# Optimization experiments

Hardware: AMD Instinct MI355X
Metric: run time of the kernel (lower is better)

## Reference

```python
import jax, jax.numpy as jnp
import numpy as np

# decoded layout constants
NN, NO, SD = 16, 8, 4          # num_neighbors, num_obstacles, state_dim_per_agent
B = 131072                      # batch rows
H1, E, HP, AD = 64, 16, 64, 2   # phi hidden, embed, psi hidden, action dim
D_ROBOT, D_OBST = 0.3, 0.3
B_GAMMA, B_EXPH = 0.05, 1.0
PHI_MIN, PHI_MAX = -2.0, 2.0
A_MAX = 2.0


def setup_inputs() -> dict:
    key = jax.random.key(0)
    kx, kw = jax.random.split(key)
    # x: [count | goal(SD) | NN neighbor rel-states (SD each) | NO obstacle rel-pos (2 each)]
    x = jax.random.normal(kx, (B, 1 + SD + SD * NN + 2 * NO), dtype=jnp.float32) * 2.0
    x = x.at[:, 0].set(float(NN))
    names = [("Wp1n", (SD, H1)), ("bp1n", (H1,)), ("Wp2n", (H1, E)), ("bp2n", (E,)),
             ("Wr1n", (E, H1)), ("br1n", (H1,)), ("Wr2n", (H1, E)), ("br2n", (E,)),
             ("Wp1o", (2, H1)), ("bp1o", (H1,)), ("Wp2o", (H1, E)), ("bp2o", (E,)),
             ("Wr1o", (E, H1)), ("br1o", (H1,)), ("Wr2o", (H1, E)), ("br2o", (E,)),
             ("Wpsi1", (2 * E + SD, HP)), ("bpsi1", (HP,)), ("Wpsi2", (HP, AD)), ("bpsi2", (AD,))]
    ks = jax.random.split(kw, len(names))
    inp = {"x": x}
    for (n, sh), k in zip(names, ks):
        s = 1.0 / np.sqrt(sh[0])  # torch Linear default init scale
        inp[n] = jax.random.uniform(k, sh, jnp.float32, -s, s)
    return inp


def _mlp2(h, W1, b1, W2, b2):
    # Feedforward: activation between layers, linear output
    return jax.nn.relu(h @ W1 + b1) @ W2 + b2


def _deepset(el, Wp1, bp1, Wp2, bp2, Wr1, br1, Wr2, br2):
    # el: [B, n, d] -> phi each element, sum over set, rho
    phi = _mlp2(el, Wp1, bp1, Wp2, bp2)          # [B, n, E]
    return _mlp2(phi.sum(axis=1), Wr1, br1, Wr2, br2)  # [B, E]


def _barrier_sum(P, D):
    # P: [B, n, 2]; APF barrier gamma * P / (|P| * (|P|-D)^exph), summed over n
    nrm = jnp.linalg.norm(P, axis=-1, keepdims=True)   # [B, n, 1]
    H = nrm - D
    return (B_GAMMA * P / (nrm * H ** B_EXPH)).sum(axis=1)  # [B, 2]


def reference(x, Wp1n, bp1n, Wp2n, bp2n, Wr1n, br1n, Wr2n, br2n,
              Wp1o, bp1o, Wp2o, bp2o, Wr1o, br1o, Wr2o, br2o,
              Wpsi1, bpsi1, Wpsi2, bpsi2):
    nb = x.shape[0]
    g = x[:, 1:1 + SD]                                        # goal
    nbr = x[:, 1 + SD:1 + SD + SD * NN].reshape(nb, NN, SD)   # neighbor rel-states
    obs = x[:, 1 + SD + SD * NN:].reshape(nb, NO, 2)          # obstacle rel-pos

    rho_n = _deepset(nbr, Wp1n, bp1n, Wp2n, bp2n, Wr1n, br1n, Wr2n, br2n)
    rho_o = _deepset(obs, Wp1o, bp1o, Wp2o, bp2o, Wr1o, br1o, Wr2o, br2o)

    h = jnp.concatenate([rho_n, rho_o, g], axis=1)            # [B, 2E+SD]
    emp = _mlp2(h, Wpsi1, bpsi1, Wpsi2, bpsi2)                # psi network
    emp = (jnp.tanh(emp) + 1.0) / 2.0 * (PHI_MAX - PHI_MIN) + PHI_MIN  # scale_empty

    bar = _barrier_sum(-nbr[:, :, :2], D_ROBOT) + _barrier_sum(-obs, D_OBST)

    action = emp + bar
    # scale(): divide rows whose inf-norm exceeds a_max
    inv_alpha = jnp.maximum(jnp.max(jnp.abs(action), axis=1, keepdims=True) / A_MAX, 1.0)
    return action / inv_alpha
```

## Files before the change

kernel.cpp:

```cpp
#include <hip/hip_runtime.h>
#include <math.h>


typedef __attribute__((ext_vector_type(8))) _Float16 f16x8;
typedef __attribute__((ext_vector_type(2))) __fp16 fp16x2;
typedef __attribute__((ext_vector_type(4))) float f32x4;

#define XW 85

#define FR_S1N  0
#define FR_S1O  4
#define FR_FN   8
#define FR_FO   16
#define FR_ZN   24
#define FR_ZO   32
#define FR_WG   40
#define FR_PSI2 44
#define FR_SPN  46
#define FR_SPO  50
#define N_FRAGS 54

#define BIG_STR 144
#define L_BIG  0
#define L_BIG2 2304
#define L_OUT  4608
#define L_BAR  4736
#define GRP_LDS 4864
#define NBA_STR 136

#define H16_ONE 0x00003C00u

__device__ __forceinline__ float fast_rcp(float x)  { return __builtin_amdgcn_rcpf(x); }
__device__ __forceinline__ float fast_sqrt(float x) { return __builtin_amdgcn_sqrtf(x); }

__device__ __forceinline__ float two_tanh(float a) {
    float ax = fabsf(a);
    float e = __expf(2.0f * ax);
    float t = 1.0f - 2.0f * fast_rcp(e + 1.0f);
    return copysignf(2.0f * t, a);
}

__device__ __forceinline__ void lds_order() {
    __asm__ __volatile__("" ::: "memory");
}

__device__ __forceinline__ unsigned pk2(float a, float b) {
    union { fp16x2 h; unsigned u; } t;
    t.h = __builtin_amdgcn_cvt_pkrtz(a, b);
    return t.u;
}
__device__ __forceinline__ f16x8 lds_af(const char* area, int stride, int off, int lane) {
    int mm = lane & 15, qq = lane >> 4;
    return *(const f16x8*)(area + mm * stride + off + qq * 16);
}
__device__ __forceinline__ f16x8 load_bh(const _Float16* wsf, int frag, int lane) {
    return ((const f16x8*)(wsf + (size_t)frag * 512))[lane];
}
__device__ __forceinline__ f32x4 cinit(float b) {
    f32x4 c; c[0] = b; c[1] = b; c[2] = b; c[3] = b; return c;
}
__device__ __forceinline__ f32x4 mfma1(f16x8 a, f16x8 b, f32x4 c) {
    return __builtin_amdgcn_mfma_f32_16x16x32_f16(a, b, c, 0, 0, 0);
}

__global__ void bn_prep(const float* __restrict__ Wp1n, const float* __restrict__ Wp2n,
                        const float* __restrict__ Wr1n, const float* __restrict__ Wr2n,
                        const float* __restrict__ Wp1o, const float* __restrict__ Wp2o,
                        const float* __restrict__ Wr1o, const float* __restrict__ Wr2o,
                        const float* __restrict__ Wpsi1, const float* __restrict__ Wpsi2,
                        const float* __restrict__ bp1n, const float* __restrict__ bp1o,
                        const float* __restrict__ bp2n, const float* __restrict__ bp2o,
                        const float* __restrict__ br1n, const float* __restrict__ br1o,
                        const float* __restrict__ br2n, const float* __restrict__ br2o,
                        const float* __restrict__ bpsi1,
                        _Float16* __restrict__ wsf)
{
    int f = blockIdx.x;
    int lane = threadIdx.x;
    int q = lane >> 4, c = lane & 15;

    if (f >= N_FRAGS) {
        float* dst = (float*)(wsf + (size_t)N_FRAGS * 512) + (f - N_FRAGS) * 64;
        if (lane < 64) {
            if (f == N_FRAGS) {
                float s = 0.f;
                for (int e = 0; e < 16; ++e) s = fmaf(bp2n[e], Wr1n[e * 64 + lane], s);
                dst[lane] = 16.f * s + br1n[lane];
            } else if (f == N_FRAGS + 1) {
                float s = 0.f;
                for (int e = 0; e < 16; ++e) s = fmaf(bp2o[e], Wr1o[e * 64 + lane], s);
                dst[lane] = 8.f * s + br1o[lane];
            } else if (f == N_FRAGS + 2) {
                dst[lane] = 16.f * bp1n[lane];
            } else {
                dst[lane] = 8.f * bp1o[lane];
            }
        }
        return;
    }

    _Float16* dstf = wsf + (size_t)f * 512 + lane * 8;

    if (f < 8) {
        const float* W   = (f < 4) ? Wp1n : Wp1o;
        const float* bia = (f < 4) ? bp1n : bp1o;
        int K  = (f < 4) ? 4 : 2;
        int nt = f & 3;
        for (int j = 0; j < 8; ++j) {
            int k = q * 8 + j;
            int n = nt * 16 + c;
            float v = 0.f;
            if (k < K) v = W[k * 64 + n];
            else if (k == K) v = bia[n];
            dstf[j] = (_Float16)v;
        }
    } else if (f < 24) {
        int rel = (f - 8) & 7;
        bool isN = f < 16;
        const float* Wa = isN ? Wp2n : Wp2o;
        const float* Wb = isN ? Wr1n : Wr1o;
        int kk = rel >> 2, nt = rel & 3;
        for (int j = 0; j < 8; ++j) {
            int k = kk * 32 + q * 8 + j;
            int n = nt * 16 + c;
            float s = 0.f;
            for (int e = 0; e < 16; ++e) s = fmaf(Wa[k * 16 + e], Wb[e * 64 + n], s);
            dstf[j] = (_Float16)(0.5f * s);
        }
    } else if (f < 40) {
        int rel = (f - 24) & 7;
        bool isN = f < 32;
        const float* Wa = isN ? Wr2n : Wr2o;
        int roff = isN ? 0 : 16;
        int kk = rel >> 2, nt = rel & 3;
        for (int j = 0; j < 8; ++j) {
            int k = kk * 32 + q * 8 + j;
            int n = nt * 16 + c;
            float s = 0.f;
            for (int e = 0; e < 16; ++e) s = fmaf(Wa[k * 16 + e], Wpsi1[(roff + e) * 64 + n], s);
            dstf[j] = (_Float16)s;
        }
    } else if (f < 44) {
        int nt = f - 40;
        for (int j = 0; j < 8; ++j) {
            int k = q * 8 + j;
            int n = nt * 16 + c;
            float v = 0.f;
            if (k < 4) v = Wpsi1[(32 + k) * 64 + n];
            else if (k == 4) {
                float s = bpsi1[n];
                for (int e = 0; e < 16; ++e) {
                    s = fmaf(br2n[e], Wpsi1[e * 64 + n], s);
                    s = fmaf(br2o[e], Wpsi1[(16 + e) * 64 + n], s);
                }
                v = s;
            }
            dstf[j] = (_Float16)v;
        }
    } else if (f < 46) {
        int kk = f - 44;
        for (int j = 0; j < 8; ++j) {
            int k = kk * 32 + q * 8 + j;
            float v = (c < 2) ? Wpsi2[k * 2 + c] : 0.f;
            dstf[j] = (_Float16)v;
        }
    } else if (f < 50) {
        int nt = f - 46;
        for (int j = 0; j < 8; ++j) {
            int k = q * 8 + j;
            int n = nt * 16 + c;
            dstf[j] = (_Float16)Wp1n[(k & 3) * 64 + n];
        }
    } else {
        int nt = f - 50;
        for (int j = 0; j < 8; ++j) {
            int k = q * 8 + j;
            int n = nt * 16 + c;
            float v = (k < 16) ? Wp1o[(k & 1) * 64 + n] : 0.f;
            dstf[j] = (_Float16)v;
        }
    }
}

__global__ __launch_bounds__(256, 5) void bn_main(
    const float* __restrict__ x, const _Float16* __restrict__ wsf,
    const float* __restrict__ bpsi2,
    float* __restrict__ out, int nb)
{
    __shared__ char smem[4 * GRP_LDS];
    const int lane = threadIdx.x & 63;
    const int wid  = threadIdx.x >> 6;
    const int group = blockIdx.x * 4 + wid;
    const int row0 = group * 16;

    char* Gl   = smem + wid * GRP_LDS;
    char* BIG  = Gl + L_BIG;
    char* BIG2 = Gl + L_BIG2;
    char* OUTA = Gl + L_OUT;
    char* BAR  = Gl + L_BAR;
    char* NBA  = BIG;

    const int m = lane & 15, q = lane >> 4, c = m;
    const float* xg   = x + (size_t)row0 * XW;
    const float* xrow = xg + (size_t)m * XW;

    const float* BFN = (const float*)(wsf + (size_t)N_FRAGS * 512);
    const float* BFO = BFN + 64;
    const float* BSN = BFN + 128;
    const float* BSO = BFN + 192;

    const f32x4 ZC = cinit(0.f);

    {
        int ln5 = lane >> 5;
        int pr  = lane & 31;
        int mm0 = pr >> 1, fp = pr & 1;
        char* db = NBA + mm0 * NBA_STR + fp * 4;
        const float* s0 = xg + (size_t)ln5 * XW + 5 + pr * 2;
        #pragma unroll
        for (int t = 0; t < 8; ++t) {
            const float* s = s0 + (size_t)(2 * t) * XW;
            *(unsigned*)(db + (2 * t + ln5) * 8) = pk2(s[0], s[1]);
        }
    }

    union { f16x8 v; unsigned u[4]; } gA;
    gA.u[0] = pk2(xrow[1], xrow[2]);
    gA.u[1] = pk2(xrow[3], xrow[4]);
    gA.u[2] = H16_ONE;
    gA.u[3] = 0;

    unsigned obs[8];
    #pragma unroll
    for (int t = 0; t < 8; ++t)
        obs[t] = pk2(xrow[69 + 2 * t], xrow[70 + 2 * t]);

    {
        float bx = 0.f, by = 0.f;
        #pragma unroll
        for (int i = 0; i < 4; ++i) {
            int n = 4 * q + i;
            float px = -xrow[5 + 4 * n], py = -xrow[6 + 4 * n];
            float nrm = fast_sqrt(px * px + py * py);
            float coef = 0.05f * fast_rcp(nrm * (nrm - 0.3f));
            bx = fmaf(coef, px, bx);
            by = fmaf(coef, py, by);
        }
        #pragma unroll
        for (int i = 0; i < 2; ++i) {
            int o = 2 * q + i;
            float px = -xrow[69 + 2 * o], py = -xrow[70 + 2 * o];
            float nrm = fast_sqrt(px * px + py * py);
            float coef = 0.05f * fast_rcp(nrm * (nrm - 0.3f));
            bx = fmaf(coef, px, bx);
            by = fmaf(coef, py, by);
        }
        bx += __shfl_xor(bx, 16); by += __shfl_xor(by, 16);
        bx += __shfl_xor(bx, 32); by += __shfl_xor(by, 32);
        if (q == 0) { float2 bb; bb.x = bx; bb.y = by; *(float2*)(BAR + m * 8) = bb; }
    }

    {
        f16x8 Bspo[4], Bs1o[4];
        #pragma unroll
        for (int nt = 0; nt < 4; ++nt) {
            Bspo[nt] = load_bh(wsf, FR_SPO + nt, lane);
            Bs1o[nt] = load_bh(wsf, FR_S1O + nt, lane);
        }
        union { f16x8 v; unsigned u[4]; } Apo;
        Apo.u[0] = q == 0 ? obs[0] : (q == 1 ? obs[4] : 0u);
        Apo.u[1] = q == 0 ? obs[1] : (q == 1 ? obs[5] : 0u);
        Apo.u[2] = q == 0 ? obs[2] : (q == 1 ? obs[6] : 0u);
        Apo.u[3] = q == 0 ? obs[3] : (q == 1 ? obs[7] : 0u);

        f32x4 accS[4], accA[4];
        #pragma unroll
        for (int nt = 0; nt < 4; ++nt) {
            accS[nt] = mfma1(Apo.v, Bspo[nt], cinit(BSO[nt * 16 + c]));
            accA[nt] = cinit(0.f);
        }
        union { f16x8 v; unsigned u[4]; } A;
        A.u[1] = H16_ONE; A.u[2] = 0; A.u[3] = 0;
        #pragma unroll
        for (int oo = 0; oo < 8; ++oo) {
            A.u[0] = obs[oo];
            #pragma unroll
            for (int nt = 0; nt < 4; ++nt) {
                f32x4 cc = mfma1(A.v, Bs1o[nt], ZC);
                #pragma unroll
                for (int reg = 0; reg < 4; ++reg)
                    accA[nt][reg] += fabsf(cc[reg]);
            }
        }
        #pragma unroll
        for (int nt = 0; nt < 4; ++nt)
            #pragma unroll
            for (int reg = 0; reg < 4; ++reg)
                *(_Float16*)(BIG2 + (q * 4 + reg) * BIG_STR + (nt * 16 + c) * 2)
                    = (_Float16)(accS[nt][reg] + accA[nt][reg]);
    }
    lds_order();

    {
        f16x8 Bspn[4], Bs1n[4];
        #pragma unroll
        for (int nt = 0; nt < 4; ++nt) {
            Bspn[nt] = load_bh(wsf, FR_SPN + nt, lane);
            Bs1n[nt] = load_bh(wsf, FR_S1N + nt, lane);
        }
        const int m8 = m * 8;
        union { f16x8 v; uint2 h[2]; } Ap0, Ap1;
        Ap0.h[0] = *(const uint2*)(NBA + (2 * q) * NBA_STR + m8);
        Ap0.h[1] = *(const uint2*)(NBA + (2 * q + 1) * NBA_STR + m8);
        Ap1.h[0] = *(const uint2*)(NBA + (2 * q + 8) * NBA_STR + m8);
        Ap1.h[1] = *(const uint2*)(NBA + (2 * q + 9) * NBA_STR + m8);

        f32x4 accS[4], accA[4];
        #pragma unroll
        for (int nt = 0; nt < 4; ++nt) {
            accS[nt] = mfma1(Ap1.v, Bspn[nt],
                       mfma1(Ap0.v, Bspn[nt], cinit(BSN[nt * 16 + c])));
            accA[nt] = cinit(0.f);
        }
        union { f16x8 v; unsigned u[4]; uint2 h[2]; } A;
        A.u[2] = H16_ONE; A.u[3] = 0;
        #pragma unroll
        for (int mm = 0; mm < 16; ++mm) {
            A.h[0] = *(const uint2*)(NBA + mm * NBA_STR + m8);
            #pragma unroll
            for (int nt = 0; nt < 4; ++nt) {
                f32x4 cc = mfma1(A.v, Bs1n[nt], ZC);
                #pragma unroll
                for (int reg = 0; reg < 4; ++reg)
                    accA[nt][reg] += fabsf(cc[reg]);
            }
        }
        lds_order();
        #pragma unroll
        for (int nt = 0; nt < 4; ++nt)
            #pragma unroll
            for (int reg = 0; reg < 4; ++reg)
                *(_Float16*)(BIG + (q * 4 + reg) * BIG_STR + (nt * 16 + c) * 2)
                    = (_Float16)(accS[nt][reg] + accA[nt][reg]);
    }
    lds_order();

    {
        f16x8 An0 = lds_af(BIG,  BIG_STR, 0, lane);
        f16x8 An1 = lds_af(BIG,  BIG_STR, 64, lane);
        f16x8 Ao0 = lds_af(BIG2, BIG_STR, 0, lane);
        f16x8 Ao1 = lds_af(BIG2, BIG_STR, 64, lane);
        #pragma unroll
        for (int nt = 0; nt < 4; ++nt) {
            f16x8 Bn0 = load_bh(wsf, FR_FN + nt, lane);
            f16x8 Bn1 = load_bh(wsf, FR_FN + 4 + nt, lane);
            f32x4 cn = mfma1(An0, Bn0, cinit(BFN[nt * 16 + c]));
            cn = mfma1(An1, Bn1, cn);
            f16x8 Bo0 = load_bh(wsf, FR_FO + nt, lane);
            f16x8 Bo1 = load_bh(wsf, FR_FO + 4 + nt, lane);
            f32x4 co = mfma1(Ao0, Bo0, cinit(BFO[nt * 16 + c]));
            co = mfma1(Ao1, Bo1, co);
            #pragma unroll
            for (int reg = 0; reg < 4; ++reg) {
                *(_Float16*)(BIG + (q * 4 + reg) * BIG_STR + (nt * 16 + c) * 2)
                    = (_Float16)fmaxf(cn[reg], 0.f);
                *(_Float16*)(BIG2 + (q * 4 + reg) * BIG_STR + (nt * 16 + c) * 2)
                    = (_Float16)fmaxf(co[reg], 0.f);
            }
        }
    }
    lds_order();

    {
        f16x8 An0 = lds_af(BIG,  BIG_STR, 0, lane);
        f16x8 An1 = lds_af(BIG,  BIG_STR, 64, lane);
        f16x8 Ao0 = lds_af(BIG2, BIG_STR, 0, lane);
        f16x8 Ao1 = lds_af(BIG2, BIG_STR, 64, lane);
        #pragma unroll
        for (int nt = 0; nt < 4; ++nt) {
            f16x8 Bg  = load_bh(wsf, FR_WG + nt, lane);
            f16x8 Bn0 = load_bh(wsf, FR_ZN + nt, lane);
            f16x8 Bn1 = load_bh(wsf, FR_ZN + 4 + nt, lane);
            f16x8 Bo0 = load_bh(wsf, FR_ZO + nt, lane);
            f16x8 Bo1 = load_bh(wsf, FR_ZO + 4 + nt, lane);
            f32x4 cc = mfma1(gA.v, Bg, ZC);
            cc = mfma1(An0, Bn0, cc);
            cc = mfma1(An1, Bn1, cc);
            cc = mfma1(Ao0, Bo0, cc);
            cc = mfma1(Ao1, Bo1, cc);
            #pragma unroll
            for (int reg = 0; reg < 4; ++reg)
                *(_Float16*)(BIG + (q * 4 + reg) * BIG_STR + (nt * 16 + c) * 2)
                    = (_Float16)fmaxf(cc[reg], 0.f);
        }
    }
    lds_order();

    {
        float b_p2 = (c < 2) ? bpsi2[c] : 0.f;
        f16x8 Bp20 = load_bh(wsf, FR_PSI2 + 0, lane);
        f16x8 Bp21 = load_bh(wsf, FR_PSI2 + 1, lane);
        f16x8 A0 = lds_af(BIG, BIG_STR, 0, lane);
        f16x8 A1 = lds_af(BIG, BIG_STR, 64, lane);
        f32x4 ca = mfma1(A0, Bp20, cinit(b_p2));
        f32x4 cb = mfma1(A1, Bp21, ZC);
        if (c < 2) {
            #pragma unroll
            for (int reg = 0; reg < 4; ++reg)
                *(float*)(OUTA + (q * 4 + reg) * 8 + c * 4) = ca[reg] + cb[reg];
        }
    }
    lds_order();

    if (lane < 16) {
        float2 a  = *(const float2*)(OUTA + lane * 8);
        float2 bb = *(const float2*)(BAR + lane * 8);
        float a0 = two_tanh(a.x) + bb.x;
        float a1 = two_tanh(a.y) + bb.y;
        float amax = fmaxf(fabsf(a0), fabsf(a1));
        float inv_alpha = fmaxf(amax * 0.5f, 1.0f);
        float rr = fast_rcp(inv_alpha);
        float2 o; o.x = a0 * rr; o.y = a1 * rr;
        *(float2*)(out + (size_t)(row0 + lane) * 2) = o;
    }
}

extern "C" void kernel_launch(void* const* d_in, const int* in_sizes, int n_in,
                              void* d_out, int out_size, void* d_ws, size_t ws_size,
                              hipStream_t stream) {
    const float* x     = (const float*)d_in[0];
    const float* Wp1n  = (const float*)d_in[1];
    const float* bp1n  = (const float*)d_in[2];
    const float* Wp2n  = (const float*)d_in[3];
    const float* bp2n  = (const float*)d_in[4];
    const float* Wr1n  = (const float*)d_in[5];
    const float* br1n  = (const float*)d_in[6];
    const float* Wr2n  = (const float*)d_in[7];
    const float* br2n  = (const float*)d_in[8];
    const float* Wp1o  = (const float*)d_in[9];
    const float* bp1o  = (const float*)d_in[10];
    const float* Wp2o  = (const float*)d_in[11];
    const float* bp2o  = (const float*)d_in[12];
    const float* Wr1o  = (const float*)d_in[13];
    const float* br1o  = (const float*)d_in[14];
    const float* Wr2o  = (const float*)d_in[15];
    const float* br2o  = (const float*)d_in[16];
    const float* Wpsi1 = (const float*)d_in[17];
    const float* bpsi1 = (const float*)d_in[18];
    const float* Wpsi2 = (const float*)d_in[19];
    const float* bpsi2 = (const float*)d_in[20];
    float* out = (float*)d_out;

    int nb = in_sizes[0] / XW;
    _Float16* wsf = (_Float16*)d_ws;

    bn_prep<<<N_FRAGS + 4, 64, 0, stream>>>(Wp1n, Wp2n, Wr1n, Wr2n,
                                            Wp1o, Wp2o, Wr1o, Wr2o,
                                            Wpsi1, Wpsi2,
                                            bp1n, bp1o, bp2n, bp2o,
                                            br1n, br1o, br2n, br2o,
                                            bpsi1, wsf);

    int groups = (nb + 15) / 16;
    int blocks = (groups + 3) / 4;
    bn_main<<<blocks, 256, 0, stream>>>(x, wsf, bpsi2, out, nb);
}
```

Measured before the change: 138.1 us.

## Process two 16-row groups per wave to reuse weight fragments and add ILP

Each wavefront now handles two 16-row groups, so weight fragments loaded from global memory serve both groups and the independent MFMA chains interleave. The per-block tile grows to 8 groups and launch bounds drop from 5 to 4 waves per SIMD to make room for the extra registers. The linear part of the set sums is now accumulated with one extra MFMA per element, replacing the separate precomputed summed-weight fragments. That doubles the MFMA count in the set loops in exchange for fewer fragment loads. Occupancy and register pressure may get worse.

```diff
diff --git a/kernel.cpp b/kernel.cpp
--- a/kernel.cpp
+++ b/kernel.cpp
@@ -182,32 +182,34 @@
     }
 }
 
-__global__ __launch_bounds__(256, 5) void bn_main(
+__global__ __launch_bounds__(256, 4) void bn_main(
     const float* __restrict__ x, const _Float16* __restrict__ wsf,
     const float* __restrict__ bpsi2,
     float* __restrict__ out, int nb)
 {
-    __shared__ char smem[4 * GRP_LDS];
+    __shared__ char smem[8 * GRP_LDS];
     const int lane = threadIdx.x & 63;
     const int wid  = threadIdx.x >> 6;
-    const int group = blockIdx.x * 4 + wid;
-    const int row0 = group * 16;
-
-    char* Gl   = smem + wid * GRP_LDS;
-    char* BIG  = Gl + L_BIG;
-    char* BIG2 = Gl + L_BIG2;
-    char* OUTA = Gl + L_OUT;
-    char* BAR  = Gl + L_BAR;
-    char* NBA  = BIG;
+    const int g0   = blockIdx.x * 8 + wid * 2;
+    const int row0 = g0 * 16;
+    const int row1 = row0 + 16;
+
+    char* Gl0  = smem + (wid * 2) * GRP_LDS;
+    char* Gl1  = Gl0 + GRP_LDS;
+    char* BIG0 = Gl0 + L_BIG;   char* BIG1 = Gl1 + L_BIG;
+    char* BG20 = Gl0 + L_BIG2;  char* BG21 = Gl1 + L_BIG2;
+    char* OUT0 = Gl0 + L_OUT;   char* OUT1 = Gl1 + L_OUT;
+    char* BAR0 = Gl0 + L_BAR;   char* BAR1 = Gl1 + L_BAR;
+    char* NBA0 = BIG0;          char* NBA1 = BIG1;
 
     const int m = lane & 15, q = lane >> 4, c = m;
-    const float* xg   = x + (size_t)row0 * XW;
-    const float* xrow = xg + (size_t)m * XW;
+    const float* xg0   = x + (size_t)row0 * XW;
+    const float* xg1   = x + (size_t)row1 * XW;
+    const float* xrow0 = xg0 + (size_t)m * XW;
+    const float* xrow1 = xg1 + (size_t)m * XW;
 
     const float* BFN = (const float*)(wsf + (size_t)N_FRAGS * 512);
     const float* BFO = BFN + 64;
-    const float* BSN = BFN + 128;
-    const float* BSO = BFN + 192;
 
     const f32x4 ZC = cinit(0.f);
 
@@ -215,167 +217,198 @@
         int ln5 = lane >> 5;
         int pr  = lane & 31;
         int mm0 = pr >> 1, fp = pr & 1;
-        char* db = NBA + mm0 * NBA_STR + fp * 4;
-        const float* s0 = xg + (size_t)ln5 * XW + 5 + pr * 2;
+        int dbo = mm0 * NBA_STR + fp * 4;
+        const float* s00 = xg0 + (size_t)ln5 * XW + 5 + pr * 2;
+        const float* s10 = xg1 + (size_t)ln5 * XW + 5 + pr * 2;
         #pragma unroll
         for (int t = 0; t < 8; ++t) {
-            const float* s = s0 + (size_t)(2 * t) * XW;
-            *(unsigned*)(db + (2 * t + ln5) * 8) = pk2(s[0], s[1]);
-        }
-    }
-
-    union { f16x8 v; unsigned u[4]; } gA;
-    gA.u[0] = pk2(xrow[1], xrow[2]);
-    gA.u[1] = pk2(xrow[3], xrow[4]);
-    gA.u[2] = H16_ONE;
-    gA.u[3] = 0;
-
-    unsigned obs[8];
+            const float* sa = s00 + (size_t)(2 * t) * XW;
+            const float* sb = s10 + (size_t)(2 * t) * XW;
+            *(unsigned*)(NBA0 + dbo + (2 * t + ln5) * 8) = pk2(sa[0], sa[1]);
+            *(unsigned*)(NBA1 + dbo + (2 * t + ln5) * 8) = pk2(sb[0], sb[1]);
+        }
+    }
+
+    union { f16x8 v; unsigned u[4]; } gA0, gA1;
+    gA0.u[0] = pk2(xrow0[1], xrow0[2]);
+    gA0.u[1] = pk2(xrow0[3], xrow0[4]);
+    gA0.u[2] = H16_ONE; gA0.u[3] = 0;
+    gA1.u[0] = pk2(xrow1[1], xrow1[2]);
+    gA1.u[1] = pk2(xrow1[3], xrow1[4]);
+    gA1.u[2] = H16_ONE; gA1.u[3] = 0;
+
+    unsigned obs0[8], obs1[8];
     #pragma unroll
-    for (int t = 0; t < 8; ++t)
-        obs[t] = pk2(xrow[69 + 2 * t], xrow[70 + 2 * t]);
-
-    {
-        float bx = 0.f, by = 0.f;
+    for (int t = 0; t < 8; ++t) {
+        obs0[t] = pk2(xrow0[69 + 2 * t], xrow0[70 + 2 * t]);
+        obs1[t] = pk2(xrow1[69 + 2 * t], xrow1[70 + 2 * t]);
+    }
+
+    {
+        float bx0 = 0.f, by0 = 0.f, bx1 = 0.f, by1 = 0.f;
         #pragma unroll
         for (int i = 0; i < 4; ++i) {
             int n = 4 * q + i;
-            float px = -xrow[5 + 4 * n], py = -xrow[6 + 4 * n];
-            float nrm = fast_sqrt(px * px + py * py);
-            float coef = 0.05f * fast_rcp(nrm * (nrm - 0.3f));
-            bx = fmaf(coef, px, bx);
-            by = fmaf(coef, py, by);
+            float p0x = -xrow0[5 + 4 * n], p0y = -xrow0[6 + 4 * n];
+            float n0 = fast_sqrt(p0x * p0x + p0y * p0y);
+            float c0 = 0.05f * fast_rcp(n0 * (n0 - 0.3f));
+            bx0 = fmaf(c0, p0x, bx0); by0 = fmaf(c0, p0y, by0);
+            float p1x = -xrow1[5 + 4 * n], p1y = -xrow1[6 + 4 * n];
+            float n1 = fast_sqrt(p1x * p1x + p1y * p1y);
+            float c1 = 0.05f * fast_rcp(n1 * (n1 - 0.3f));
+            bx1 = fmaf(c1, p1x, bx1); by1 = fmaf(c1, p1y, by1);
         }
         #pragma unroll
         for (int i = 0; i < 2; ++i) {
             int o = 2 * q + i;
-            float px = -xrow[69 + 2 * o], py = -xrow[70 + 2 * o];
-            float nrm = fast_sqrt(px * px + py * py);
-            float coef = 0.05f * fast_rcp(nrm * (nrm - 0.3f));
-            bx = fmaf(coef, px, bx);
-            by = fmaf(coef, py, by);
-        }
-        bx += __shfl_xor(bx, 16); by += __shfl_xor(by, 16);
-        bx += __shfl_xor(bx, 32); by += __shfl_xor(by, 32);
-        if (q == 0) { float2 bb; bb.x = bx; bb.y = by; *(float2*)(BAR + m * 8) = bb; }
-    }
-
-    {
-        f16x8 Bspo[4], Bs1o[4];
+            float p0x = -xrow0[69 + 2 * o], p0y = -xrow0[70 + 2 * o];
+            float n0 = fast_sqrt(p0x * p0x + p0y * p0y);
+            float c0 = 0.05f * fast_rcp(n0 * (n0 - 0.3f));
+            bx0 = fmaf(c0, p0x, bx0); by0 = fmaf(c0, p0y, by0);
+            float p1x = -xrow1[69 + 2 * o], p1y = -xrow1[70 + 2 * o];
+            float n1 = fast_sqrt(p1x * p1x + p1y * p1y);
+            float c1 = 0.05f * fast_rcp(n1 * (n1 - 0.3f));
+            bx1 = fmaf(c1, p1x, bx1); by1 = fmaf(c1, p1y, by1);
+        }
+        bx0 += __shfl_xor(bx0, 16); by0 += __shfl_xor(by0, 16);
+        bx0 += __shfl_xor(bx0, 32); by0 += __shfl_xor(by0, 32);
+        bx1 += __shfl_xor(bx1, 16); by1 += __shfl_xor(by1, 16);
+        bx1 += __shfl_xor(bx1, 32); by1 += __shfl_xor(by1, 32);
+        if (q == 0) {
+            float2 b0; b0.x = bx0; b0.y = by0; *(float2*)(BAR0 + m * 8) = b0;
+            float2 b1; b1.x = bx1; b1.y = by1; *(float2*)(BAR1 + m * 8) = b1;
+        }
+    }
+
+    {
+        f16x8 Bs1o[4];
+        #pragma unroll
+        for (int nt = 0; nt < 4; ++nt) Bs1o[nt] = load_bh(wsf, FR_S1O + nt, lane);
+
+        f32x4 aS0[4], aA0[4], aS1[4], aA1[4];
         #pragma unroll
         for (int nt = 0; nt < 4; ++nt) {
-            Bspo[nt] = load_bh(wsf, FR_SPO + nt, lane);
-            Bs1o[nt] = load_bh(wsf, FR_S1O + nt, lane);
-        }
-        union { f16x8 v; unsigned u[4]; } Apo;
-        Apo.u[0] = q == 0 ? obs[0] : (q == 1 ? obs[4] : 0u);
-        Apo.u[1] = q == 0 ? obs[1] : (q == 1 ? obs[5] : 0u);
-        Apo.u[2] = q == 0 ? obs[2] : (q == 1 ? obs[6] : 0u);
-        Apo.u[3] = q == 0 ? obs[3] : (q == 1 ? obs[7] : 0u);
-
-        f32x4 accS[4], accA[4];
+            aS0[nt] = cinit(0.f); aA0[nt] = cinit(0.f);
+            aS1[nt] = cinit(0.f); aA1[nt] = cinit(0.f);
+        }
+        union { f16x8 v; unsigned u[4]; } A0, A1;
+        A0.u[1] = H16_ONE; A0.u[2] = 0; A0.u[3] = 0;
+        A1.u[1] = H16_ONE; A1.u[2] = 0; A1.u[3] = 0;
+        #pragma unroll
+        for (int oo = 0; oo < 8; ++oo) {
+            A0.u[0] = obs0[oo];
+            A1.u[0] = obs1[oo];
+            #pragma unroll
+            for (int nt = 0; nt < 4; ++nt) {
+                aS0[nt] = mfma1(A0.v, Bs1o[nt], aS0[nt]);
+                f32x4 c0 = mfma1(A0.v, Bs1o[nt], ZC);
+                aS1[nt] = mfma1(A1.v, Bs1o[nt], aS1[nt]);
+                f32x4 c1 = mfma1(A1.v, Bs1o[nt], ZC);
+                #pragma unroll
+                for (int reg = 0; reg < 4; ++reg) {
+                    aA0[nt][reg] += fabsf(c0[reg]);
+                    aA1[nt][reg] += fabsf(c1[reg]);
+                }
+            }
+        }
+        #pragma unroll
+        for (int nt = 0; nt < 4; ++nt)
+            #pragma unroll
+            for (int reg = 0; reg < 4; ++reg) {
+                *(_Float16*)(BG20 + (q * 4 + reg) * BIG_STR + (nt * 16 + c) * 2)
+                    = (_Float16)(aS0[nt][reg] + aA0[nt][reg]);
+                *(_Float16*)(BG21 + (q * 4 + reg) * BIG_STR + (nt * 16 + c) * 2)
+                    = (_Float16)(aS1[nt][reg] + aA1[nt][reg]);
+            }
+    }
+    lds_order();
+
+    {
+        f16x8 Bs1n[4];
+        #pragma unroll
+        for (int nt = 0; nt < 4; ++nt) Bs1n[nt] = load_bh(wsf, FR_S1N + nt, lane);
+
+        const int m8 = m * 8;
+        f32x4 aS0[4], aA0[4], aS1[4], aA1[4];
         #pragma unroll
         for (int nt = 0; nt < 4; ++nt) {
-            accS[nt] = mfma1(Apo.v, Bspo[nt], cinit(BSO[nt * 16 + c]));
-            accA[nt] = cinit(0.f);
-        }
-        union { f16x8 v; unsigned u[4]; } A;
-        A.u[1] = H16_ONE; A.u[2] = 0; A.u[3] = 0;
-        #pragma unroll
-        for (int oo = 0; oo < 8; ++oo) {
-            A.u[0] = obs[oo];
+            aS0[nt] = cinit(0.f); aA0[nt] = cinit(0.f);
+            aS1[nt] = cinit(0.f); aA1[nt] = cinit(0.f);
+        }
+        union { f16x8 v; unsigned u[4]; uint2 h[2]; } A0, A1;
+        A0.u[2] = H16_ONE; A0.u[3] = 0;
+        A1.u[2] = H16_ONE; A1.u[3] = 0;
+        #pragma unroll
+        for (int mm = 0; mm < 16; ++mm) {
+            A0.h[0] = *(const uint2*)(NBA0 + mm * NBA_STR + m8);
+            A1.h[0] = *(const uint2*)(NBA1 + mm * NBA_STR + m8);
             #pragma unroll
             for (int nt = 0; nt < 4; ++nt) {
-                f32x4 cc = mfma1(A.v, Bs1o[nt], ZC);
+                aS0[nt] = mfma1(A0.v, Bs1n[nt], aS0[nt]);
+                f32x4 c0 = mfma1(A0.v, Bs1n[nt], ZC);
+                aS1[nt] = mfma1(A1.v, Bs1n[nt], aS1[nt]);
+                f32x4 c1 = mfma1(A1.v, Bs1n[nt], ZC);
                 #pragma unroll
-                for (int reg = 0; reg < 4; ++reg)
-                    accA[nt][reg] += fabsf(cc[reg]);
-            }
-        }
+                for (int reg = 0; reg < 4; ++reg) {
+                    aA0[nt][reg] += fabsf(c0[reg]);
+                    aA1[nt][reg] += fabsf(c1[reg]);
+                }
+            }
+        }
+        lds_order();
         #pragma unroll
         for (int nt = 0; nt < 4; ++nt)
             #pragma unroll
-            for (int reg = 0; reg < 4; ++reg)
-                *(_Float16*)(BIG2 + (q * 4 + reg) * BIG_STR + (nt * 16 + c) * 2)
-                    = (_Float16)(accS[nt][reg] + accA[nt][reg]);
+            for (int reg = 0; reg < 4; ++reg) {
+                *(_Float16*)(BIG0 + (q * 4 + reg) * BIG_STR + (nt * 16 + c) * 2)
+                    = (_Float16)(aS0[nt][reg] + aA0[nt][reg]);
+                *(_Float16*)(BIG1 + (q * 4 + reg) * BIG_STR + (nt * 16 + c) * 2)
+                    = (_Float16)(aS1[nt][reg] + aA1[nt][reg]);
+            }
     }
     lds_order();
 
     {
-        f16x8 Bspn[4], Bs1n[4];
-        #pragma unroll
-        for (int nt = 0; nt < 4; ++nt) {
-            Bspn[nt] = load_bh(wsf, FR_SPN + nt, lane);
-            Bs1n[nt] = load_bh(wsf, FR_S1N + nt, lane);
-        }
-        const int m8 = m * 8;
-        union { f16x8 v; uint2 h[2]; } Ap0, Ap1;
-        Ap0.h[0] = *(const uint2*)(NBA + (2 * q) * NBA_STR + m8);
-        Ap0.h[1] = *(const uint2*)(NBA + (2 * q + 1) * NBA_STR + m8);
-        Ap1.h[0] = *(const uint2*)(NBA + (2 * q + 8) * NBA_STR + m8);
-        Ap1.h[1] = *(const uint2*)(NBA + (2 * q + 9) * NBA_STR + m8);
-
-        f32x4 accS[4], accA[4];
-        #pragma unroll
-        for (int nt = 0; nt < 4; ++nt) {
-            accS[nt] = mfma1(Ap1.v, Bspn[nt],
-                       mfma1(Ap0.v, Bspn[nt], cinit(BSN[nt * 16 + c])));
-            accA[nt] = cinit(0.f);
-        }
-        union { f16x8 v; unsigned u[4]; uint2 h[2]; } A;
-        A.u[2] = H16_ONE; A.u[3] = 0;
-        #pragma unroll
-        for (int mm = 0; mm < 16; ++mm) {
-            A.h[0] = *(const uint2*)(NBA + mm * NBA_STR + m8);
-            #pragma unroll
-            for (int nt = 0; nt < 4; ++nt) {
-                f32x4 cc = mfma1(A.v, Bs1n[nt], ZC);
-                #pragma unroll
-                for (int reg = 0; reg < 4; ++reg)
-                    accA[nt][reg] += fabsf(cc[reg]);
-            }
-        }
-        lds_order();
-        #pragma unroll
-        for (int nt = 0; nt < 4; ++nt)
-            #pragma unroll
-            for (int reg = 0; reg < 4; ++reg)
-                *(_Float16*)(BIG + (q * 4 + reg) * BIG_STR + (nt * 16 + c) * 2)
-                    = (_Float16)(accS[nt][reg] + accA[nt][reg]);
-    }
-    lds_order();
-
-    {
-        f16x8 An0 = lds_af(BIG,  BIG_STR, 0, lane);
-        f16x8 An1 = lds_af(BIG,  BIG_STR, 64, lane);
-        f16x8 Ao0 = lds_af(BIG2, BIG_STR, 0, lane);
-        f16x8 Ao1 = lds_af(BIG2, BIG_STR, 64, lane);
+        f16x8 An00 = lds_af(BIG0, BIG_STR, 0, lane);
+        f16x8 An01 = lds_af(BIG0, BIG_STR, 64, lane);
+        f16x8 Ao00 = lds_af(BG20, BIG_STR, 0, lane);
+        f16x8 Ao01 = lds_af(BG20, BIG_STR, 64, lane);
+        f16x8 An10 = lds_af(BIG1, BIG_STR, 0, lane);
+        f16x8 An11 = lds_af(BIG1, BIG_STR, 64, lane);
+        f16x8 Ao10 = lds_af(BG21, BIG_STR, 0, lane);
+        f16x8 Ao11 = lds_af(BG21, BIG_STR, 64, lane);
         #pragma unroll
         for (int nt = 0; nt < 4; ++nt) {
             f16x8 Bn0 = load_bh(wsf, FR_FN + nt, lane);
             f16x8 Bn1 = load_bh(wsf, FR_FN + 4 + nt, lane);
-            f32x4 cn = mfma1(An0, Bn0, cinit(BFN[nt * 16 + c]));
-            cn = mfma1(An1, Bn1, cn);
             f16x8 Bo0 = load_bh(wsf, FR_FO + nt, lane);
             f16x8 Bo1 = load_bh(wsf, FR_FO + 4 + nt, lane);
-            f32x4 co = mfma1(Ao0, Bo0, cinit(BFO[nt * 16 + c]));
-            co = mfma1(Ao1, Bo1, co);
+            float bfn = BFN[nt * 16 + c], bfo = BFO[nt * 16 + c];
+            f32x4 cn0 = mfma1(An01, Bn1, mfma1(An00, Bn0, cinit(bfn)));
+            f32x4 co0 = mfma1(Ao01, Bo1, mfma1(Ao00, Bo0, cinit(bfo)));
+            f32x4 cn1 = mfma1(An11, Bn1, mfma1(An10, Bn0, cinit(bfn)));
+            f32x4 co1 = mfma1(Ao11, Bo1, mfma1(Ao10, Bo0, cinit(bfo)));
             #pragma unroll
             for (int reg = 0; reg < 4; ++reg) {
-                *(_Float16*)(BIG + (q * 4 + reg) * BIG_STR + (nt * 16 + c) * 2)
-                    = (_Float16)fmaxf(cn[reg], 0.f);
-                *(_Float16*)(BIG2 + (q * 4 + reg) * BIG_STR + (nt * 16 + c) * 2)
-                    = (_Float16)fmaxf(co[reg], 0.f);
+                int off = (q * 4 + reg) * BIG_STR + (nt * 16 + c) * 2;
+                *(_Float16*)(BIG0 + off) = (_Float16)fmaxf(cn0[reg], 0.f);
+                *(_Float16*)(BG20 + off) = (_Float16)fmaxf(co0[reg], 0.f);
+                *(_Float16*)(BIG1 + off) = (_Float16)fmaxf(cn1[reg], 0.f);
+                *(_Float16*)(BG21 + off) = (_Float16)fmaxf(co1[reg], 0.f);
             }
         }
     }
     lds_order();
 
     {
-        f16x8 An0 = lds_af(BIG,  BIG_STR, 0, lane);
-        f16x8 An1 = lds_af(BIG,  BIG_STR, 64, lane);
-        f16x8 Ao0 = lds_af(BIG2, BIG_STR, 0, lane);
-        f16x8 Ao1 = lds_af(BIG2, BIG_STR, 64, lane);
+        f16x8 An00 = lds_af(BIG0, BIG_STR, 0, lane);
+        f16x8 An01 = lds_af(BIG0, BIG_STR, 64, lane);
+        f16x8 Ao00 = lds_af(BG20, BIG_STR, 0, lane);
+        f16x8 Ao01 = lds_af(BG20, BIG_STR, 64, lane);
+        f16x8 An10 = lds_af(BIG1, BIG_STR, 0, lane);
+        f16x8 An11 = lds_af(BIG1, BIG_STR, 64, lane);
+        f16x8 Ao10 = lds_af(BG21, BIG_STR, 0, lane);
+        f16x8 Ao11 = lds_af(BG21, BIG_STR, 64, lane);
         #pragma unroll
         for (int nt = 0; nt < 4; ++nt) {
             f16x8 Bg  = load_bh(wsf, FR_WG + nt, lane);
@@ -383,15 +416,22 @@
             f16x8 Bn1 = load_bh(wsf, FR_ZN + 4 + nt, lane);
             f16x8 Bo0 = load_bh(wsf, FR_ZO + nt, lane);
             f16x8 Bo1 = load_bh(wsf, FR_ZO + 4 + nt, lane);
-            f32x4 cc = mfma1(gA.v, Bg, ZC);
-            cc = mfma1(An0, Bn0, cc);
-            cc = mfma1(An1, Bn1, cc);
-            cc = mfma1(Ao0, Bo0, cc);
-            cc = mfma1(Ao1, Bo1, cc);
-            #pragma unroll
-            for (int reg = 0; reg < 4; ++reg)
-                *(_Float16*)(BIG + (q * 4 + reg) * BIG_STR + (nt * 16 + c) * 2)
-                    = (_Float16)fmaxf(cc[reg], 0.f);
+            f32x4 c0 = mfma1(gA0.v, Bg, ZC);
+            c0 = mfma1(An00, Bn0, c0);
+            c0 = mfma1(An01, Bn1, c0);
+            c0 = mfma1(Ao00, Bo0, c0);
+            c0 = mfma1(Ao01, Bo1, c0);
+            f32x4 c1 = mfma1(gA1.v, Bg, ZC);
+            c1 = mfma1(An10, Bn0, c1);
+            c1 = mfma1(An11, Bn1, c1);
+            c1 = mfma1(Ao10, Bo0, c1);
+            c1 = mfma1(Ao11, Bo1, c1);
+            #pragma unroll
+            for (int reg = 0; reg < 4; ++reg) {
+                int off = (q * 4 + reg) * BIG_STR + (nt * 16 + c) * 2;
+                *(_Float16*)(BIG0 + off) = (_Float16)fmaxf(c0[reg], 0.f);
+                *(_Float16*)(BIG1 + off) = (_Float16)fmaxf(c1[reg], 0.f);
+            }
         }
     }
     lds_order();
@@ -400,28 +440,40 @@
         float b_p2 = (c < 2) ? bpsi2[c] : 0.f;
         f16x8 Bp20 = load_bh(wsf, FR_PSI2 + 0, lane);
         f16x8 Bp21 = load_bh(wsf, FR_PSI2 + 1, lane);
-        f16x8 A0 = lds_af(BIG, BIG_STR, 0, lane);
-        f16x8 A1 = lds_af(BIG, BIG_STR, 64, lane);
-        f32x4 ca = mfma1(A0, Bp20, cinit(b_p2));
-        f32x4 cb = mfma1(A1, Bp21, ZC);
+        f16x8 A00 = lds_af(BIG0, BIG_STR, 0, lane);
+        f16x8 A01 = lds_af(BIG0, BIG_STR, 64, lane);
+        f16x8 A10 = lds_af(BIG1, BIG_STR, 0, lane);
+        f16x8 A11 = lds_af(BIG1, BIG_STR, 64, lane);
+        f32x4 c0 = mfma1(A01, Bp21, mfma1(A00, Bp20, cinit(b_p2)));
+        f32x4 c1 = mfma1(A11, Bp21, mfma1(A10, Bp20, cinit(b_p2)));
         if (c < 2) {
             #pragma unroll
-            for (int reg = 0; reg < 4; ++reg)
-                *(float*)(OUTA + (q * 4 + reg) * 8 + c * 4) = ca[reg] + cb[reg];
+            for (int reg = 0; reg < 4; ++reg) {
+                *(float*)(OUT0 + (q * 4 + reg) * 8 + c * 4) = c0[reg];
+                *(float*)(OUT1 + (q * 4 + reg) * 8 + c * 4) = c1[reg];
+            }
         }
     }
     lds_order();
 
     if (lane < 16) {
-        float2 a  = *(const float2*)(OUTA + lane * 8);
-        float2 bb = *(const float2*)(BAR + lane * 8);
-        float a0 = two_tanh(a.x) + bb.x;
-        float a1 = two_tanh(a.y) + bb.y;
-        float amax = fmaxf(fabsf(a0), fabsf(a1));
-        float inv_alpha = fmaxf(amax * 0.5f, 1.0f);
-        float rr = fast_rcp(inv_alpha);
-        float2 o; o.x = a0 * rr; o.y = a1 * rr;
-        *(float2*)(out + (size_t)(row0 + lane) * 2) = o;
+        float2 a0 = *(const float2*)(OUT0 + lane * 8);
+        float2 b0 = *(const float2*)(BAR0 + lane * 8);
+        float u0 = two_tanh(a0.x) + b0.x;
+        float v0 = two_tanh(a0.y) + b0.y;
+        float ia0 = fmaxf(fmaxf(fabsf(u0), fabsf(v0)) * 0.5f, 1.0f);
+        float r0 = fast_rcp(ia0);
+        float2 o0; o0.x = u0 * r0; o0.y = v0 * r0;
+        *(float2*)(out + (size_t)(row0 + lane) * 2) = o0;
+
+        float2 a1 = *(const float2*)(OUT1 + lane * 8);
+        float2 b1 = *(const float2*)(BAR1 + lane * 8);
+        float u1 = two_tanh(a1.x) + b1.x;
+        float v1 = two_tanh(a1.y) + b1.y;
+        float ia1 = fmaxf(fmaxf(fabsf(u1), fabsf(v1)) * 0.5f, 1.0f);
+        float r1 = fast_rcp(ia1);
+        float2 o1; o1.x = u1 * r1; o1.y = v1 * r1;
+        *(float2*)(out + (size_t)(row1 + lane) * 2) = o1;
     }
 }
 
@@ -462,6 +514,6 @@
                                             bpsi1, wsf);
 
     int groups = (nb + 15) / 16;
-    int blocks = (groups + 3) / 4;
+    int blocks = (groups + 7) / 8;
     bn_main<<<blocks, 256, 0, stream>>>(x, wsf, bpsi2, out, nb);
 }
```

After: 150.8 us. +9.2%, slower.
